# Kernel optimization log

Measured on AMD Instinct MI355X. Metric: run time of the kernel, lower is better.

The kernel has to match this reference:

```python
import jax, jax.numpy as jnp
import numpy as np

N_NODES = 100000
N_EDGES = 3200000
N_GRAPHS = 256
HID = 32
IN_DIM = 6
BN_EPS = 1e-5


def setup_inputs() -> dict:
    key = jax.random.key(0)
    ks = jax.random.split(key, 24)
    inp = {}
    inp['x'] = jax.random.normal(ks[0], (N_NODES, IN_DIM), dtype=jnp.float32)
    inp['edge_index'] = jax.random.randint(ks[1], (2, N_EDGES), 0, N_NODES)
    inp['pos'] = jax.random.normal(ks[2], (N_NODES, 6), dtype=jnp.float32)
    inp['batch'] = jnp.sort(jax.random.randint(ks[3], (N_NODES,), 0, N_GRAPHS))
    # GaussKernel params
    inp['inv_sigma1'] = jax.random.uniform(ks[4], (1,)) * 0.02 + 0.99
    inp['inv_sigma2'] = jax.random.uniform(ks[5], (1,)) * 0.02 + 0.99
    # GCNConv weights (glorot-ish scale) + biases
    dims = [IN_DIM, HID, HID, HID, HID]
    for i in range(4):
        s = 1.0 / np.sqrt(dims[i])
        inp[f'W{i+1}'] = jax.random.normal(ks[6 + i], (dims[i], dims[i + 1]), dtype=jnp.float32) * s
        inp[f'b{i+1}'] = jnp.zeros((dims[i + 1],), dtype=jnp.float32)
    # BatchNorm (layers 1..3 only; last layer has no BN) - eval mode params
    for i in range(3):
        inp[f'g{i+1}'] = jnp.ones((HID,), dtype=jnp.float32)
        inp[f'be{i+1}'] = jnp.zeros((HID,), dtype=jnp.float32)
    # post-MP linear HID -> 1
    inp['Wout'] = jax.random.normal(ks[20], (HID, 1), dtype=jnp.float32) * (1.0 / np.sqrt(HID))
    inp['bout'] = jnp.zeros((1,), dtype=jnp.float32)
    return inp


def _gauss_kernel(pos, row, col, s1, s2):
    p1, p2 = pos[row, :3], pos[col, :3]
    a1, a2 = pos[row, 3:], pos[col, 3:]
    D = jnp.sum((p1 - p2) ** 2, axis=-1)               # [E]
    T = (1.0 - jnp.sum(a1 * a2, axis=-1)) ** 2         # [E]
    return jnp.exp(-(D * s1[0] ** 2 + T * s2[0] ** 2))  # [E]


def _gcn_conv(x, W, b, row, col, ew):
    # PyG GCNConv (normalize=True, add_self_loops=True, fill_value=1.0)
    n = x.shape[0]
    xw = x @ W                                          # [N, out]
    deg = jnp.zeros((n,), xw.dtype).at[col].add(ew) + 1.0  # self-loop weight 1
    dinv = jnp.where(deg > 0, deg ** -0.5, 0.0)
    norm = dinv[row] * ew * dinv[col]                   # [E]
    out = jnp.zeros_like(xw).at[col].add(norm[:, None] * xw[row])
    out = out + (dinv * dinv)[:, None] * xw             # self-loop messages
    return out + b


def _bn_eval(x, g, be):
    # running_mean=0, running_var=1 at init (inference mode)
    return x * (g / jnp.sqrt(1.0 + BN_EPS)) + be


def reference(x, edge_index, pos, batch, inv_sigma1, inv_sigma2,
              W1, b1, W2, b2, W3, b3, W4, b4,
              g1, be1, g2, be2, g3, be3, Wout, bout):
    row, col = edge_index[0], edge_index[1]
    ew = _gauss_kernel(pos, row, col, inv_sigma1, inv_sigma2)
    # layer 1..3: GCN -> BN -> ReLU (dropout is identity in eval)
    h = x
    for (W, b, g, be) in ((W1, b1, g1, be1), (W2, b2, g2, be2), (W3, b3, g3, be3)):
        h = _gcn_conv(h, W, b, row, col, ew)
        h = jax.nn.relu(_bn_eval(h, g, be))
    # layer 4: plain GCN (no BN / act / dropout)
    h = _gcn_conv(h, W4, b4, row, col, ew)
    emb = h
    # graph task: global mean pool then Linear + Sigmoid
    sums = jax.ops.segment_sum(h, batch, num_segments=N_GRAPHS)
    cnts = jax.ops.segment_sum(jnp.ones((h.shape[0],), h.dtype), batch, num_segments=N_GRAPHS)
    pooled = sums / jnp.maximum(cnts, 1.0)[:, None]
    pred = jax.nn.sigmoid(pooled @ Wout + bout)
    return (emb, pred)
```

## Files before the change

### kernel.cpp

```cpp
#include <hip/hip_runtime.h>
#include <hip/hip_bf16.h>
#include <math.h>

#define TB 256
#define PCHUNK 1024
#define SLOTS 72
#define NPB 64
#define NSHARD 8
#define BCAPS 384
#define CPAD 16

struct RecPtrs { unsigned* p[NSHARD]; };

__device__ __forceinline__ void atomic_add_f32(float* p, float v) {
    unsafeAtomicAdd(p, v);
}

__device__ __forceinline__ unsigned short f2bf(float x) {
    unsigned u = __float_as_uint(x);
    return (unsigned short)((u + 0x7FFF + ((u >> 16) & 1)) >> 16);
}
__device__ __forceinline__ float4 bf4(ushort4 u) {
    return make_float4(__uint_as_float((unsigned)u.x << 16),
                       __uint_as_float((unsigned)u.y << 16),
                       __uint_as_float((unsigned)u.z << 16),
                       __uint_as_float((unsigned)u.w << 16));
}

__global__ __launch_bounds__(TB) void zero_pack_kernel(int* __restrict__ bcnt,
                                                       float* __restrict__ sums,
                                                       float* __restrict__ cnt,
                                                       const float2* __restrict__ pos2,
                                                       float4* __restrict__ pos8,
                                                       int n_nodes, int n_cnt) {
    int i = blockIdx.x * TB + threadIdx.x;
    if (i < n_nodes) {
        float2 a = pos2[i * 3 + 0], b = pos2[i * 3 + 1], c = pos2[i * 3 + 2];
        pos8[i * 2 + 0] = make_float4(a.x, a.y, b.x, b.y);
        pos8[i * 2 + 1] = make_float4(c.x, c.y, 0.f, 0.f);
    }
    if (i < n_cnt) {
        int4* bp = (int4*)bcnt + (size_t)i * 4;
        int4 z = make_int4(0, 0, 0, 0);
        bp[0] = z; bp[1] = z; bp[2] = z; bp[3] = z;
    }
    if (i < 256 * 32) sums[i] = 0.0f;
    if (i < 256) cnt[i] = 0.0f;
}

__global__ __launch_bounds__(TB) void bin_shard_kernel(
    const int* __restrict__ row, const int* __restrict__ col,
    int* __restrict__ bcnt, RecPtrs recs, int nb, int n_edges) {
    int e = blockIdx.x * TB + threadIdx.x;
    if (e >= n_edges) return;
    int shard = blockIdx.x & (NSHARD - 1);
    int r = __builtin_nontemporal_load(&row[e]);
    int c = __builtin_nontemporal_load(&col[e]);
    int b = c >> 6;
    unsigned rec = (unsigned)r | ((unsigned)(c & (NPB - 1)) << 17);
    int rank = atomicAdd(&bcnt[(size_t)(shard * nb + b) * CPAD], 1);
    if (rank < BCAPS)
        recs.p[shard][(size_t)b * BCAPS + rank] = rec;
}

__global__ __launch_bounds__(TB) void build_kernel(
    RecPtrs recs, const int* __restrict__ bcnt, const float4* __restrict__ pos8,
    const float* __restrict__ s1p, const float* __restrict__ s2p,
    int* __restrict__ hist, float* __restrict__ dinv,
    int2* __restrict__ csr, int nb, int n_nodes) {
    __shared__ float4 cpos[NPB * 2];
    __shared__ int lhist[NPB];
    __shared__ float lwsum[NPB];
    int b = blockIdx.x, tid = threadIdx.x;
    int cbase = b << 6;
    if (tid < NPB) { lhist[tid] = 0; lwsum[tid] = 0.0f; }
    if (tid < NPB * 2) {
        int node = cbase + (tid >> 1);
        if (node < n_nodes) cpos[tid] = pos8[(size_t)node * 2 + (tid & 1)];
    }
    __syncthreads();
    float s1 = s1p[0], s2 = s2p[0];
    int wv = tid >> 6, ln = tid & 63;
    for (int s = wv; s < NSHARD; s += 4) {
        int cnt_s = min(bcnt[(size_t)(s * nb + b) * CPAD], BCAPS);
        const unsigned* rp = recs.p[s] + (size_t)b * BCAPS;
        for (int e = ln; e < cnt_s; e += 64) {
            unsigned rec = __builtin_nontemporal_load(&rp[e]);
            int r = (int)(rec & 0x1FFFFu);
            int cl = (int)((rec >> 17) & (NPB - 1));
            float4 ra = pos8[(size_t)r * 2 + 0], rb = pos8[(size_t)r * 2 + 1];
            float4 ca = cpos[cl * 2 + 0], cb = cpos[cl * 2 + 1];
            float dx = ra.x - ca.x, dy = ra.y - ca.y, dz = ra.z - ca.z;
            float D = dx * dx + dy * dy + dz * dz;
            float dot = ra.w * ca.w + rb.x * cb.x + rb.y * cb.y;
            float t = 1.0f - dot;
            float w = expf(-(D * s1 * s1 + t * t * s2 * s2));
            int rank = atomicAdd(&lhist[cl], 1);
            atomicAdd(&lwsum[cl], w);
            if (rank < SLOTS)
                csr[(size_t)(cbase + cl) * SLOTS + rank] = make_int2(r, __float_as_int(w));
        }
    }
    __syncthreads();
    if (tid < NPB) {
        int c = cbase + tid;
        if (c < n_nodes) {
            int cnt = min(lhist[tid], SLOTS);
            hist[c] = cnt;
            dinv[c] = rsqrtf(lwsum[tid] + 1.0f);
            int nseg = (cnt + 7) >> 3;
            size_t base = (size_t)c * SLOTS;
            for (int j = cnt; j < nseg * 8; j++) csr[base + j] = make_int2(0, 0);
        }
    }
}

template <int K, bool BN>
__global__ __launch_bounds__(TB) void matmul_kernel(
    const float* __restrict__ fin, const float* __restrict__ W,
    const float* __restrict__ g, const float* __restrict__ be,
    const float* __restrict__ dinv, unsigned short* __restrict__ ywb,
    int n_nodes) {
    __shared__ float Ws[K * 32];
    __shared__ float gs[32];
    __shared__ float bs[32];
    int tid = threadIdx.x;
    for (int i = tid; i < K * 32; i += TB) Ws[i] = W[i];
    if (BN && tid < 32) {
        gs[tid] = g[tid] * (1.0f / sqrtf(1.0f + 1e-5f));
        bs[tid] = be[tid];
    }
    __syncthreads();
    int n = blockIdx.x * TB + tid;
    if (n >= n_nodes) return;
    float vals[K];
    const float* fp = fin + (size_t)n * K;
    if (K % 4 == 0) {
#pragma unroll
        for (int k = 0; k < K / 4; k++) {
            float4 v = ((const float4*)fp)[k];
            vals[k * 4 + 0] = v.x;
            vals[k * 4 + 1] = v.y;
            vals[k * 4 + 2] = v.z;
            vals[k * 4 + 3] = v.w;
        }
    } else {
#pragma unroll
        for (int k = 0; k < K; k++) vals[k] = fp[k];
    }
    if (BN) {
#pragma unroll
        for (int k = 0; k < K; k++) vals[k] = fmaxf(fmaf(vals[k], gs[k], bs[k]), 0.0f);
    }
    float acc[32];
#pragma unroll
    for (int j = 0; j < 32; j++) acc[j] = 0.0f;
#pragma unroll
    for (int k = 0; k < K; k++) {
        float v = vals[k];
#pragma unroll
        for (int j = 0; j < 32; j++) acc[j] = fmaf(v, Ws[k * 32 + j], acc[j]);
    }
    float di = dinv[n];
    uint4* op = (uint4*)(ywb + (size_t)n * 32);
#pragma unroll
    for (int j = 0; j < 4; j++) {
        uint4 pk;
        pk.x = (unsigned)f2bf(di * acc[j * 8 + 0]) | ((unsigned)f2bf(di * acc[j * 8 + 1]) << 16);
        pk.y = (unsigned)f2bf(di * acc[j * 8 + 2]) | ((unsigned)f2bf(di * acc[j * 8 + 3]) << 16);
        pk.z = (unsigned)f2bf(di * acc[j * 8 + 4]) | ((unsigned)f2bf(di * acc[j * 8 + 5]) << 16);
        pk.w = (unsigned)f2bf(di * acc[j * 8 + 6]) | ((unsigned)f2bf(di * acc[j * 8 + 7]) << 16);
        op[j] = pk;
    }
}

__device__ __forceinline__ float4 f4_fma(float w, float4 v, float4 a) {
    return make_float4(fmaf(w, v.x, a.x), fmaf(w, v.y, a.y),
                       fmaf(w, v.z, a.z), fmaf(w, v.w, a.w));
}

__device__ __forceinline__ float4 gather_core(
    const int* __restrict__ hist, const int2* __restrict__ csr,
    const unsigned short* __restrict__ ywb, int n, int lane) {
    int o = lane >> 3, f4i = (lane & 7) * 4;
    int nseg = (min(hist[n], SLOTS) + 7) >> 3;
    size_t base = (size_t)n * SLOTS;
    float4 acc = make_float4(0.f, 0.f, 0.f, 0.f);
    for (int seg = o; seg < nseg; seg += 4) {
        const int4* q = (const int4*)(csr + base + (size_t)seg * 8);
        int4 q0 = q[0], q1 = q[1], q2 = q[2], q3 = q[3];
        ushort4 u0 = *(const ushort4*)(ywb + ((size_t)q0.x << 5) + f4i);
        ushort4 u1 = *(const ushort4*)(ywb + ((size_t)q0.z << 5) + f4i);
        ushort4 u2 = *(const ushort4*)(ywb + ((size_t)q1.x << 5) + f4i);
        ushort4 u3 = *(const ushort4*)(ywb + ((size_t)q1.z << 5) + f4i);
        ushort4 u4 = *(const ushort4*)(ywb + ((size_t)q2.x << 5) + f4i);
        ushort4 u5 = *(const ushort4*)(ywb + ((size_t)q2.z << 5) + f4i);
        ushort4 u6 = *(const ushort4*)(ywb + ((size_t)q3.x << 5) + f4i);
        ushort4 u7 = *(const ushort4*)(ywb + ((size_t)q3.z << 5) + f4i);
        acc = f4_fma(__int_as_float(q0.y), bf4(u0), acc);
        acc = f4_fma(__int_as_float(q0.w), bf4(u1), acc);
        acc = f4_fma(__int_as_float(q1.y), bf4(u2), acc);
        acc = f4_fma(__int_as_float(q1.w), bf4(u3), acc);
        acc = f4_fma(__int_as_float(q2.y), bf4(u4), acc);
        acc = f4_fma(__int_as_float(q2.w), bf4(u5), acc);
        acc = f4_fma(__int_as_float(q3.y), bf4(u6), acc);
        acc = f4_fma(__int_as_float(q3.w), bf4(u7), acc);
    }
    float4 t;
    t.x = __shfl_xor(acc.x, 8, 32); t.y = __shfl_xor(acc.y, 8, 32);
    t.z = __shfl_xor(acc.z, 8, 32); t.w = __shfl_xor(acc.w, 8, 32);
    acc.x += t.x; acc.y += t.y; acc.z += t.z; acc.w += t.w;
    t.x = __shfl_xor(acc.x, 16, 32); t.y = __shfl_xor(acc.y, 16, 32);
    t.z = __shfl_xor(acc.z, 16, 32); t.w = __shfl_xor(acc.w, 16, 32);
    acc.x += t.x; acc.y += t.y; acc.z += t.z; acc.w += t.w;
    return acc;
}

__global__ __launch_bounds__(TB) void fused_layer_kernel(
    const int* __restrict__ hist, const int2* __restrict__ csr,
    const unsigned short* __restrict__ ywb_in, const float* __restrict__ dinv,
    const float4* __restrict__ bias4, const float* __restrict__ g,
    const float* __restrict__ be, const float* __restrict__ W,
    unsigned short* __restrict__ ywb_out, int n_nodes) {
    __shared__ float Ws[32 * 32];
    __shared__ float gs[32];
    __shared__ float bs[32];
    int tid = threadIdx.x;
    for (int i = tid; i < 32 * 32; i += TB) Ws[i] = W[i];
    if (tid < 32) {
        gs[tid] = g[tid] * (1.0f / sqrtf(1.0f + 1e-5f));
        bs[tid] = be[tid];
    }
    __syncthreads();
    int n = blockIdx.x * (TB / 32) + (tid >> 5);
    if (n >= n_nodes) return;
    int lane = tid & 31, f4i = (lane & 7) * 4;
    float4 acc = gather_core(hist, csr, ywb_in, n, lane);
    float di = dinv[n];
    ushort4 us = *(const ushort4*)(ywb_in + ((size_t)n << 5) + f4i);
    float4 self = bf4(us);
    float4 bb = bias4[f4i >> 2];
    float4 h;
    h.x = fmaf(di, acc.x + self.x, bb.x);
    h.y = fmaf(di, acc.y + self.y, bb.y);
    h.z = fmaf(di, acc.z + self.z, bb.z);
    h.w = fmaf(di, acc.w + self.w, bb.w);
    h.x = fmaxf(fmaf(h.x, gs[f4i + 0], bs[f4i + 0]), 0.0f);
    h.y = fmaxf(fmaf(h.y, gs[f4i + 1], bs[f4i + 1]), 0.0f);
    h.z = fmaxf(fmaf(h.z, gs[f4i + 2], bs[f4i + 2]), 0.0f);
    h.w = fmaxf(fmaf(h.w, gs[f4i + 3], bs[f4i + 3]), 0.0f);
    float y = 0.0f;
#pragma unroll
    for (int q = 0; q < 8; q++) {
        float hx = __shfl(h.x, q, 32);
        float hy = __shfl(h.y, q, 32);
        float hz = __shfl(h.z, q, 32);
        float hw = __shfl(h.w, q, 32);
        y = fmaf(hx, Ws[(4 * q + 0) * 32 + lane], y);
        y = fmaf(hy, Ws[(4 * q + 1) * 32 + lane], y);
        y = fmaf(hz, Ws[(4 * q + 2) * 32 + lane], y);
        y = fmaf(hw, Ws[(4 * q + 3) * 32 + lane], y);
    }
    ywb_out[(size_t)n * 32 + lane] = f2bf(di * y);
}

__global__ __launch_bounds__(TB) void gather_node_kernel(
    const int* __restrict__ hist, const int2* __restrict__ csr,
    const unsigned short* __restrict__ ywb, const float* __restrict__ dinv,
    const float4* __restrict__ bias4, float* __restrict__ agg, int n_nodes) {
    int n = blockIdx.x * (TB / 32) + (threadIdx.x >> 5);
    if (n >= n_nodes) return;
    int lane = threadIdx.x & 31;
    int o = lane >> 3, f4i = (lane & 7) * 4;
    float4 acc = gather_core(hist, csr, ywb, n, lane);
    if (o == 0) {
        float di = dinv[n];
        ushort4 us = *(const ushort4*)(ywb + ((size_t)n << 5) + f4i);
        float4 self = bf4(us);
        float4 bb = bias4[f4i >> 2];
        float4 v;
        v.x = fmaf(di, acc.x + self.x, bb.x);
        v.y = fmaf(di, acc.y + self.y, bb.y);
        v.z = fmaf(di, acc.z + self.z, bb.z);
        v.w = fmaf(di, acc.w + self.w, bb.w);
        ((float4*)agg)[(size_t)n * 8 + (f4i >> 2)] = v;
    }
}

__global__ __launch_bounds__(TB) void pool_kernel(
    const float* __restrict__ agg, const int* __restrict__ batch,
    float* __restrict__ sums, float* __restrict__ cnt, int n_nodes) {
    int j = threadIdx.x & 31;
    int s = threadIdx.x >> 5;
    int base = blockIdx.x * PCHUNK;
    int endn = min(base + PCHUNK, n_nodes);
    float acc = 0.0f;
    float cacc = 0.0f;
    int cur = -1;
    for (int n = base + s; n < endn; n += 8) {
        int bg = batch[n];
        float v = agg[(size_t)n * 32 + j];
        if (bg != cur) {
            if (cur >= 0) {
                atomic_add_f32(&sums[(size_t)cur * 32 + j], acc);
                if (j == 0) atomic_add_f32(&cnt[cur], cacc);
            }
            cur = bg; acc = 0.0f; cacc = 0.0f;
        }
        acc += v;
        cacc += 1.0f;
    }
    if (cur >= 0) {
        atomic_add_f32(&sums[(size_t)cur * 32 + j], acc);
        if (j == 0) atomic_add_f32(&cnt[cur], cacc);
    }
}

__global__ __launch_bounds__(TB) void pred_kernel(
    const float* __restrict__ sums, const float* __restrict__ cnt,
    const float* __restrict__ Wout, const float* __restrict__ bout,
    float* __restrict__ out) {
    int g = blockIdx.x * TB + threadIdx.x;
    if (g >= 256) return;
    float c = fmaxf(cnt[g], 1.0f);
    float acc = 0.0f;
#pragma unroll
    for (int j = 0; j < 32; j++) acc += sums[g * 32 + j] * Wout[j];
    float z = acc / c + bout[0];
    out[g] = 1.0f / (1.0f + expf(-z));
}

extern "C" void kernel_launch(void* const* d_in, const int* in_sizes, int n_in,
                              void* d_out, int out_size, void* d_ws, size_t ws_size,
                              hipStream_t stream) {
    const float* x = (const float*)d_in[0];
    const int* edge_index = (const int*)d_in[1];
    const float* pos = (const float*)d_in[2];
    const int* batch = (const int*)d_in[3];
    const float* s1 = (const float*)d_in[4];
    const float* s2 = (const float*)d_in[5];
    const float* W1 = (const float*)d_in[6];
    const float* b1 = (const float*)d_in[7];
    const float* W2 = (const float*)d_in[8];
    const float* b2 = (const float*)d_in[9];
    const float* W3 = (const float*)d_in[10];
    const float* b3 = (const float*)d_in[11];
    const float* W4 = (const float*)d_in[12];
    const float* b4 = (const float*)d_in[13];
    const float* g1 = (const float*)d_in[14];
    const float* be1 = (const float*)d_in[15];
    const float* g2 = (const float*)d_in[16];
    const float* be2 = (const float*)d_in[17];
    const float* g3 = (const float*)d_in[18];
    const float* be3 = (const float*)d_in[19];
    const float* Wout = (const float*)d_in[20];
    const float* bout = (const float*)d_in[21];

    const size_t E = (size_t)in_sizes[1] / 2;
    const size_t N = (size_t)in_sizes[3];

    const int* row = edge_index;
    const int* col = edge_index + E;

    const int NB = (int)((N + NPB - 1) / NPB);

    auto align256 = [](size_t v) { return (v + 255) & ~(size_t)255; };
    char* w = (char*)d_ws;
    int2* csr = (int2*)w;      w += align256(N * SLOTS * 8);
    int* hist = (int*)w;       w += align256(N * 4);
    unsigned short* ywbA = (unsigned short*)w; w += align256(N * 32 * 2);
    unsigned short* ywbB = (unsigned short*)w; w += align256(N * 32 * 2);
    float4* pos8 = (float4*)w; w += align256(N * 8 * 4);
    float* dinv = (float*)w;   w += align256(N * 4);
    float* sums = (float*)w;   w += align256(256 * 32 * 4);
    float* cnt = (float*)w;    w += align256(256 * 4);
    int* bcnt = (int*)w;       w += align256((size_t)NSHARD * NB * CPAD * 4);

    float* out_emb = (float*)d_out;
    float* out_pred = (float*)d_out + N * 32;

    const size_t SHREC = (size_t)NB * BCAPS;
    RecPtrs recs;
    for (int s = 0; s < 5; s++) recs.p[s] = (unsigned*)d_out + (size_t)s * SHREC;
    for (int s = 5; s < NSHARD; s++) recs.p[s] = (unsigned*)ywbA + (size_t)(s - 5) * SHREC;

    const int gN = (int)((N + TB - 1) / TB);
    const int gE = (int)((E + TB - 1) / TB);
    const int gW = (int)((N + (TB / 32) - 1) / (TB / 32));
    const int gP = (int)((N + PCHUNK - 1) / PCHUNK);
    const int n_cnt = NSHARD * NB;

    zero_pack_kernel<<<gN, TB, 0, stream>>>(bcnt, sums, cnt, (const float2*)pos,
                                            pos8, (int)N, n_cnt);
    bin_shard_kernel<<<gE, TB, 0, stream>>>(row, col, bcnt, recs, NB, (int)E);
    build_kernel<<<NB, TB, 0, stream>>>(recs, bcnt, pos8, s1, s2,
                                        hist, dinv, csr, NB, (int)N);

    matmul_kernel<6, false><<<gN, TB, 0, stream>>>(x, W1, nullptr, nullptr, dinv,
                                                   ywbA, (int)N);
    fused_layer_kernel<<<gW, TB, 0, stream>>>(hist, csr, ywbA, dinv,
                                              (const float4*)b1, g1, be1, W2,
                                              ywbB, (int)N);
    fused_layer_kernel<<<gW, TB, 0, stream>>>(hist, csr, ywbB, dinv,
                                              (const float4*)b2, g2, be2, W3,
                                              ywbA, (int)N);
    fused_layer_kernel<<<gW, TB, 0, stream>>>(hist, csr, ywbA, dinv,
                                              (const float4*)b3, g3, be3, W4,
                                              ywbB, (int)N);
    gather_node_kernel<<<gW, TB, 0, stream>>>(hist, csr, ywbB, dinv,
                                              (const float4*)b4, out_emb, (int)N);

    pool_kernel<<<gP, TB, 0, stream>>>(out_emb, batch, sums, cnt, (int)N);
    pred_kernel<<<1, TB, 0, stream>>>(sums, cnt, Wout, bout, out_pred);
}
```

Baseline: 514.8 us.

## Replace sharded atomic binning with count-scan-scatter counting sort of edges

```diff
diff --git a/kernel.cpp b/kernel.cpp
--- a/kernel.cpp
+++ b/kernel.cpp
@@ -3,14 +3,12 @@
 #include <math.h>
 
 #define TB 256
+#define TB_BIN 512
+#define NBLK 256
 #define PCHUNK 1024
 #define SLOTS 72
 #define NPB 64
-#define NSHARD 8
-#define BCAPS 384
-#define CPAD 16
-
-struct RecPtrs { unsigned* p[NSHARD]; };
+#define MAXNB 2048
 
 __device__ __forceinline__ void atomic_add_f32(float* p, float v) {
     unsafeAtomicAdd(p, v);
@@ -27,47 +25,105 @@
                        __uint_as_float((unsigned)u.w << 16));
 }
 
-__global__ __launch_bounds__(TB) void zero_pack_kernel(int* __restrict__ bcnt,
-                                                       float* __restrict__ sums,
+__global__ __launch_bounds__(TB) void zero_pack_kernel(float* __restrict__ sums,
                                                        float* __restrict__ cnt,
                                                        const float2* __restrict__ pos2,
                                                        float4* __restrict__ pos8,
-                                                       int n_nodes, int n_cnt) {
+                                                       int n_nodes) {
     int i = blockIdx.x * TB + threadIdx.x;
     if (i < n_nodes) {
         float2 a = pos2[i * 3 + 0], b = pos2[i * 3 + 1], c = pos2[i * 3 + 2];
         pos8[i * 2 + 0] = make_float4(a.x, a.y, b.x, b.y);
         pos8[i * 2 + 1] = make_float4(c.x, c.y, 0.f, 0.f);
     }
-    if (i < n_cnt) {
-        int4* bp = (int4*)bcnt + (size_t)i * 4;
-        int4 z = make_int4(0, 0, 0, 0);
-        bp[0] = z; bp[1] = z; bp[2] = z; bp[3] = z;
-    }
     if (i < 256 * 32) sums[i] = 0.0f;
     if (i < 256) cnt[i] = 0.0f;
 }
 
-__global__ __launch_bounds__(TB) void bin_shard_kernel(
+__global__ __launch_bounds__(TB_BIN) void count_kernel(
+    const int* __restrict__ col, int* __restrict__ blkcnt,
+    int nb, int n_edges, int chunk) {
+    __shared__ int h[MAXNB];
+    int blk = blockIdx.x, tid = threadIdx.x;
+    for (int i = tid; i < nb; i += TB_BIN) h[i] = 0;
+    __syncthreads();
+    size_t s = (size_t)blk * chunk;
+    size_t e1 = min(s + (size_t)chunk, (size_t)n_edges);
+    for (size_t e = s + tid; e < e1; e += TB_BIN) {
+        int c = __builtin_nontemporal_load(&col[e]);
+        atomicAdd(&h[c >> 6], 1);
+    }
+    __syncthreads();
+    for (int i = tid; i < nb; i += TB_BIN) blkcnt[(size_t)blk * nb + i] = h[i];
+}
+
+__global__ __launch_bounds__(TB) void scanA_kernel(
+    const int* __restrict__ blkcnt, int* __restrict__ blkpre,
+    int* __restrict__ cnt, int nb) {
+    int b = blockIdx.x * TB + threadIdx.x;
+    if (b >= nb) return;
+    int run = 0;
+#pragma unroll 4
+    for (int blk = 0; blk < NBLK; blk++) {
+        size_t idx = (size_t)blk * nb + b;
+        int v = blkcnt[idx];
+        blkpre[idx] = run;
+        run += v;
+    }
+    cnt[b] = run;
+}
+
+__global__ __launch_bounds__(TB) void scanB_kernel(
+    const int* __restrict__ cnt, int* __restrict__ off, int nb) {
+    __shared__ int part[TB];
+    int t = threadIdx.x;
+    int chunk = (nb + TB - 1) / TB;
+    int s0 = t * chunk, s1 = min(s0 + chunk, nb);
+    int s = 0;
+    for (int i = s0; i < s1; i++) s += cnt[i];
+    part[t] = s;
+    __syncthreads();
+    for (int d = 1; d < TB; d <<= 1) {
+        int v = (t >= d) ? part[t - d] : 0;
+        __syncthreads();
+        part[t] += v;
+        __syncthreads();
+    }
+    int run = (t == 0) ? 0 : part[t - 1];
+    for (int i = s0; i < s1; i++) { off[i] = run; run += cnt[i]; }
+    if (t == TB - 1) off[nb] = part[TB - 1];
+}
+
+__global__ __launch_bounds__(TB_BIN) void scatter_kernel(
     const int* __restrict__ row, const int* __restrict__ col,
-    int* __restrict__ bcnt, RecPtrs recs, int nb, int n_edges) {
-    int e = blockIdx.x * TB + threadIdx.x;
-    if (e >= n_edges) return;
-    int shard = blockIdx.x & (NSHARD - 1);
-    int r = __builtin_nontemporal_load(&row[e]);
-    int c = __builtin_nontemporal_load(&col[e]);
-    int b = c >> 6;
-    unsigned rec = (unsigned)r | ((unsigned)(c & (NPB - 1)) << 17);
-    int rank = atomicAdd(&bcnt[(size_t)(shard * nb + b) * CPAD], 1);
-    if (rank < BCAPS)
-        recs.p[shard][(size_t)b * BCAPS + rank] = rec;
+    const int* __restrict__ blkpre, const int* __restrict__ off,
+    unsigned* __restrict__ records, int nb, int n_edges, int chunk) {
+    __shared__ int base[MAXNB];
+    __shared__ int cur[MAXNB];
+    int blk = blockIdx.x, tid = threadIdx.x;
+    for (int i = tid; i < nb; i += TB_BIN) {
+        base[i] = off[i] + blkpre[(size_t)blk * nb + i];
+        cur[i] = 0;
+    }
+    __syncthreads();
+    size_t s = (size_t)blk * chunk;
+    size_t e1 = min(s + (size_t)chunk, (size_t)n_edges);
+    for (size_t e = s + tid; e < e1; e += TB_BIN) {
+        int r = __builtin_nontemporal_load(&row[e]);
+        int c = __builtin_nontemporal_load(&col[e]);
+        int bk = c >> 6;
+        int lr = atomicAdd(&cur[bk], 1);
+        unsigned rec = (unsigned)r | ((unsigned)(c & (NPB - 1)) << 17);
+        records[(size_t)base[bk] + lr] = rec;
+    }
 }
 
 __global__ __launch_bounds__(TB) void build_kernel(
-    RecPtrs recs, const int* __restrict__ bcnt, const float4* __restrict__ pos8,
+    const unsigned* __restrict__ records, const int* __restrict__ off,
+    const float4* __restrict__ pos8,
     const float* __restrict__ s1p, const float* __restrict__ s2p,
     int* __restrict__ hist, float* __restrict__ dinv,
-    int2* __restrict__ csr, int nb, int n_nodes) {
+    int2* __restrict__ csr, int n_nodes) {
     __shared__ float4 cpos[NPB * 2];
     __shared__ int lhist[NPB];
     __shared__ float lwsum[NPB];
@@ -80,26 +136,22 @@
     }
     __syncthreads();
     float s1 = s1p[0], s2 = s2p[0];
-    int wv = tid >> 6, ln = tid & 63;
-    for (int s = wv; s < NSHARD; s += 4) {
-        int cnt_s = min(bcnt[(size_t)(s * nb + b) * CPAD], BCAPS);
-        const unsigned* rp = recs.p[s] + (size_t)b * BCAPS;
-        for (int e = ln; e < cnt_s; e += 64) {
-            unsigned rec = __builtin_nontemporal_load(&rp[e]);
-            int r = (int)(rec & 0x1FFFFu);
-            int cl = (int)((rec >> 17) & (NPB - 1));
-            float4 ra = pos8[(size_t)r * 2 + 0], rb = pos8[(size_t)r * 2 + 1];
-            float4 ca = cpos[cl * 2 + 0], cb = cpos[cl * 2 + 1];
-            float dx = ra.x - ca.x, dy = ra.y - ca.y, dz = ra.z - ca.z;
-            float D = dx * dx + dy * dy + dz * dz;
-            float dot = ra.w * ca.w + rb.x * cb.x + rb.y * cb.y;
-            float t = 1.0f - dot;
-            float w = expf(-(D * s1 * s1 + t * t * s2 * s2));
-            int rank = atomicAdd(&lhist[cl], 1);
-            atomicAdd(&lwsum[cl], w);
-            if (rank < SLOTS)
-                csr[(size_t)(cbase + cl) * SLOTS + rank] = make_int2(r, __float_as_int(w));
-        }
+    int rs = off[b], re = off[b + 1];
+    for (int e = rs + tid; e < re; e += TB) {
+        unsigned rec = __builtin_nontemporal_load(&records[e]);
+        int r = (int)(rec & 0x1FFFFu);
+        int cl = (int)((rec >> 17) & (NPB - 1));
+        float4 ra = pos8[(size_t)r * 2 + 0], rb = pos8[(size_t)r * 2 + 1];
+        float4 ca = cpos[cl * 2 + 0], cb = cpos[cl * 2 + 1];
+        float dx = ra.x - ca.x, dy = ra.y - ca.y, dz = ra.z - ca.z;
+        float D = dx * dx + dy * dy + dz * dz;
+        float dot = ra.w * ca.w + rb.x * cb.x + rb.y * cb.y;
+        float t = 1.0f - dot;
+        float w = expf(-(D * s1 * s1 + t * t * s2 * s2));
+        int rank = atomicAdd(&lhist[cl], 1);
+        atomicAdd(&lwsum[cl], w);
+        if (rank < SLOTS)
+            csr[(size_t)(cbase + cl) * SLOTS + rank] = make_int2(r, __float_as_int(w));
     }
     __syncthreads();
     if (tid < NPB) {
@@ -363,6 +415,7 @@
     const int* col = edge_index + E;
 
     const int NB = (int)((N + NPB - 1) / NPB);
+    const int chunk = (int)((E + NBLK - 1) / NBLK);
 
     auto align256 = [](size_t v) { return (v + 255) & ~(size_t)255; };
     char* w = (char*)d_ws;
@@ -374,27 +427,30 @@
     float* dinv = (float*)w;   w += align256(N * 4);
     float* sums = (float*)w;   w += align256(256 * 32 * 4);
     float* cnt = (float*)w;    w += align256(256 * 4);
-    int* bcnt = (int*)w;       w += align256((size_t)NSHARD * NB * CPAD * 4);
+    int* blkcnt = (int*)w;     w += align256((size_t)NBLK * NB * 4);
+    int* blkpre = (int*)w;     w += align256((size_t)NBLK * NB * 4);
+    int* bcnt = (int*)w;       w += align256((size_t)NB * 4);
+    int* boff = (int*)w;       w += align256((size_t)(NB + 1) * 4);
 
     float* out_emb = (float*)d_out;
     float* out_pred = (float*)d_out + N * 32;
 
-    const size_t SHREC = (size_t)NB * BCAPS;
-    RecPtrs recs;
-    for (int s = 0; s < 5; s++) recs.p[s] = (unsigned*)d_out + (size_t)s * SHREC;
-    for (int s = 5; s < NSHARD; s++) recs.p[s] = (unsigned*)ywbA + (size_t)(s - 5) * SHREC;
+    unsigned* records = (unsigned*)d_out;
 
     const int gN = (int)((N + TB - 1) / TB);
-    const int gE = (int)((E + TB - 1) / TB);
     const int gW = (int)((N + (TB / 32) - 1) / (TB / 32));
     const int gP = (int)((N + PCHUNK - 1) / PCHUNK);
-    const int n_cnt = NSHARD * NB;
-
-    zero_pack_kernel<<<gN, TB, 0, stream>>>(bcnt, sums, cnt, (const float2*)pos,
-                                            pos8, (int)N, n_cnt);
-    bin_shard_kernel<<<gE, TB, 0, stream>>>(row, col, bcnt, recs, NB, (int)E);
-    build_kernel<<<NB, TB, 0, stream>>>(recs, bcnt, pos8, s1, s2,
-                                        hist, dinv, csr, NB, (int)N);
+    const int gSA = (NB + TB - 1) / TB;
+
+    zero_pack_kernel<<<gN, TB, 0, stream>>>(sums, cnt, (const float2*)pos,
+                                            pos8, (int)N);
+    count_kernel<<<NBLK, TB_BIN, 0, stream>>>(col, blkcnt, NB, (int)E, chunk);
+    scanA_kernel<<<gSA, TB, 0, stream>>>(blkcnt, blkpre, bcnt, NB);
+    scanB_kernel<<<1, TB, 0, stream>>>(bcnt, boff, NB);
+    scatter_kernel<<<NBLK, TB_BIN, 0, stream>>>(row, col, blkpre, boff,
+                                                records, NB, (int)E, chunk);
+    build_kernel<<<NB, TB, 0, stream>>>(records, boff, pos8, s1, s2,
+                                        hist, dinv, csr, (int)N);
 
     matmul_kernel<6, false><<<gN, TB, 0, stream>>>(x, W1, nullptr, nullptr, dinv,
                                                    ywbA, (int)N);
```

After: 501.3 us. 1.03x faster.
